# Performance work log

Measured on AMD Instinct MI355X. Metric: run time of the kernel, lower is better.

The kernel has to match this reference:

```python
import jax, jax.numpy as jnp
import numpy as np

NAF, NBF, DT = 64, 32, 1
B, GROUP = 2000, 100
P = B * GROUP

def _lin(key, din, dout):
    kw, kb = jax.random.split(key)
    return (jax.random.normal(kw, (din, dout), jnp.float32) * 0.02,
            jax.random.normal(kb, (dout,), jnp.float32) * 0.01)

def setup_inputs() -> dict:
    key = jax.random.key(0)
    ks = jax.random.split(key, 12)
    pairs = jax.random.normal(ks[0], (P, 2 * NAF + NBF), jnp.float32)
    idx_pairs = jnp.full((B,), GROUP, dtype=jnp.int32)
    ref_feats = jax.random.normal(ks[1], (B, 32), jnp.float32)
    aw, ab = _lin(ks[2], NAF, 128)
    bw, bb = _lin(ks[3], NBF, 128)
    p1w, p1b = _lin(ks[4], 384, 512)
    p2w, p2b = _lin(ks[5], 512, 256)
    p3w, p3b = _lin(ks[6], 256, 1024)
    f1w, f1b = _lin(ks[7], 1024, 512)
    f2w, f2b = _lin(ks[8], 512, 32)
    f3w, f3b = _lin(ks[9], 32, DT)
    return dict(pairs=pairs, idx_pairs=idx_pairs, ref_feats=ref_feats,
                aw=aw, ab=ab, bw=bw, bb=bb,
                p1w=p1w, p1b=p1b, p2w=p2w, p2b=p2b, p3w=p3w, p3b=p3b,
                f1w=f1w, f1b=f1b, f2w=f2w, f2b=f2b, f3w=f3w, f3b=f3b)

def reference(pairs, idx_pairs, ref_feats,
              aw, ab, bw, bb,
              p1w, p1b, p2w, p2b, p3w, p3b,
              f1w, f1b, f2w, f2b, f3w, f3b):
    relu = jax.nn.relu
    a1 = relu(pairs[:, :NAF] @ aw + ab)            # [P,128]
    a2 = relu(pairs[:, NAF:2 * NAF] @ aw + ab)     # [P,128]
    be = relu(pairs[:, 2 * NAF:] @ bw + bb)        # [P,128]
    h = jnp.concatenate([a1, a2, be], axis=1)      # [P,384]
    h = relu(h @ p1w + p1b)
    h = relu(h @ p2w + p2b)
    x = h @ p3w + p3b                              # [P,1024]
    nb = idx_pairs.shape[0]
    seg = jnp.repeat(jnp.arange(nb, dtype=jnp.int32), idx_pairs,
                     total_repeat_length=x.shape[0])
    sums = jax.ops.segment_sum(x, seg, num_segments=nb)
    h_pair = sums / idx_pairs[:, None].astype(x.dtype)  # segment mean [B,1024]
    h = relu(h_pair @ f1w + f1b)
    h = relu(h @ f2w + f2b)
    return h @ f3w + f3b                           # [B,1]
```

## Files before the change

kernel.cpp:

```cpp
#include <hip/hip_runtime.h>
#include <cstdint>
#include <cstddef>


typedef __bf16 bf16;
typedef __attribute__((ext_vector_type(8))) __bf16 bf16x8;
typedef __attribute__((ext_vector_type(4))) __bf16 bf16x4;
typedef __attribute__((ext_vector_type(4))) float floatx4;

#define GRP 100
#define NWIN 3125

#define WOFF_AW 0
#define WOFF_BW 8192
#define WOFF_P1 12288
#define WOFF_P2 208896
#define WOFF_P3 339968
#define WOFF_F1 602112
#define WOFF_F2 1126400
#define WOFF_HS 1142784

#define LSTR_P  168
#define LSTR_H  392
#define LSTR_H2 136
#define LSTR_MS 264

static __device__ __forceinline__ floatx4 mfma16(bf16x8 a, bf16x8 b, floatx4 c) {
  return __builtin_amdgcn_mfma_f32_16x16x32_bf16(a, b, c, 0, 0, 0);
}

static __device__ __forceinline__ void gload(floatx4& d, const bf16* p) {
  asm volatile("global_load_dwordx4 %0, %1, off" : "=v"(d) : "v"(p));
}
static __device__ __forceinline__ bf16x8 bc8(floatx4 v) {
  return __builtin_bit_cast(bf16x8, v);
}

#define VMW(N)                                         \
  do {                                                 \
    asm volatile("s_waitcnt vmcnt(" #N ")");           \
    __builtin_amdgcn_sched_barrier(0);                 \
  } while (0)

#define SYNCL()                                        \
  do {                                                 \
    asm volatile("s_waitcnt lgkmcnt(0)" ::: "memory"); \
    __builtin_amdgcn_s_barrier();                      \
  } while (0)

__global__ __launch_bounds__(256) void pack_lds(
    const float* __restrict__ aw, const float* __restrict__ bw,
    const float* __restrict__ p1w, const float* __restrict__ p2w,
    const float* __restrict__ p3w, const float* __restrict__ f1w,
    const float* __restrict__ f2w, bf16* __restrict__ wpk) {
  __shared__ float t[32][65];
  const int tid = threadIdx.x;
  int b = blockIdx.x;

  if (b < 550) {
    const float* src; int dstoff, K, N, tt;
    if (b < 4)        { src = aw;  dstoff = WOFF_AW; K = 64;   N = 128;  tt = b; }
    else if (b < 6)   { src = bw;  dstoff = WOFF_BW; K = 32;   N = 128;  tt = b - 4; }
    else if (b < 102) { src = p1w; dstoff = WOFF_P1; K = 384;  N = 512;  tt = b - 6; }
    else if (b < 166) { src = p2w; dstoff = WOFF_P2; K = 512;  N = 256;  tt = b - 102; }
    else if (b < 294) { src = p3w; dstoff = WOFF_P3; K = 256;  N = 1024; tt = b - 166; }
    else              { src = f1w; dstoff = WOFF_F1; K = 1024; N = 512;  tt = b - 294; }
    const int KT = K >> 5;
    const int kt = tt % KT;
    const int n0 = (tt / KT) * 64;
    for (int i = tid; i < 2048; i += 256) {
      int r = i >> 6, c = i & 63;
      t[r][c] = src[(size_t)(kt * 32 + r) * N + n0 + c];
    }
    __syncthreads();
    const int nc = n0 >> 7, nl0 = n0 & 127;
    bf16* dst = wpk + dstoff + ((size_t)(nc * KT + kt) * 128 + nl0) * 32;
    int o = tid * 8;
    int nl = o >> 5, kk = o & 31;
    bf16x8 v;
#pragma unroll
    for (int i = 0; i < 8; ++i) v[i] = (bf16)t[kk + i][nl];
    *(bf16x8*)(dst + nl * 32 + kk) = v;
  } else {
    const int kt = b - 550;
    for (int i = tid; i < 1024; i += 256) {
      int r = i >> 5, c = i & 31;
      t[r][c] = f2w[(size_t)(kt * 32 + r) * 32 + c];
    }
    __syncthreads();
    if (tid < 128) {
      int o = tid * 8;
      int nl = o >> 5, kk = o & 31;
      bf16x8 v;
#pragma unroll
      for (int i = 0; i < 8; ++i) v[i] = (bf16)t[kk + i][nl];
      *(bf16x8*)(wpk + WOFF_F2 + kt * 1024 + nl * 32 + kk) = v;
    }
  }
}

static __device__ __forceinline__ void kstep2(const bf16* __restrict__ Ab,
                                              int astride, int acol,
                                              const bf16* __restrict__ b0p,
                                              const bf16* __restrict__ b1p,
                                              floatx4* acc, int lm, int lq) {
  bf16x8 b0 = *(const bf16x8*)b0p;
  bf16x8 b1 = *(const bf16x8*)b1p;
#pragma unroll
  for (int mt = 0; mt < 4; ++mt) {
    bf16x8 a = *(const bf16x8*)(Ab + (mt * 16 + lm) * astride + acol + lq * 8);
    acc[mt * 2]     = mfma16(a, b0, acc[mt * 2]);
    acc[mt * 2 + 1] = mfma16(a, b1, acc[mt * 2 + 1]);
  }
}

static __device__ __forceinline__ void epi2(const floatx4* acc,
                                            const float* __restrict__ bias,
                                            bf16* dst, int dstride, int w,
                                            int lm, int lq) {
#pragma unroll
  for (int mt = 0; mt < 4; ++mt)
#pragma unroll
    for (int j = 0; j < 2; ++j) {
      int col = (w + 4 * j) * 16 + lm;
      float bv = bias[col];
      floatx4 c = acc[mt * 2 + j];
#pragma unroll
      for (int r = 0; r < 4; ++r) {
        float v = c[r] + bv;
        v = v > 0.f ? v : 0.f;
        dst[(mt * 16 + lq * 4 + r) * dstride + col] = (bf16)v;
      }
    }
}

static __device__ __forceinline__ void epi2v(const floatx4* acc, float bv0,
                                             float bv1, bf16* dst, int dstride,
                                             int w, int lm, int lq) {
#pragma unroll
  for (int mt = 0; mt < 4; ++mt)
#pragma unroll
    for (int j = 0; j < 2; ++j) {
      int col = (w + 4 * j) * 16 + lm;
      float bv = j ? bv1 : bv0;
      floatx4 c = acc[mt * 2 + j];
#pragma unroll
      for (int r = 0; r < 4; ++r) {
        float v = c[r] + bv;
        v = v > 0.f ? v : 0.f;
        dst[(mt * 16 + lq * 4 + r) * dstride + col] = (bf16)v;
      }
    }
}

__global__ __launch_bounds__(256, 2) void seg_kernel(
    const float* __restrict__ pairs, const float* __restrict__ ab,
    const float* __restrict__ bb, const float* __restrict__ p1b,
    const float* __restrict__ p2b, const bf16* __restrict__ wpk,
    float* __restrict__ hsum) {
  __shared__ __align__(16) bf16 hbuf[64 * LSTR_H];
  __shared__ __align__(16) bf16 pbuf[64 * LSTR_P];

  const int tid = threadIdx.x;
  const int w = tid >> 6;
  const int lane = tid & 63;
  const int lm = lane & 15;
  const int lq = lane >> 4;
  const int blk = blockIdx.x;

  {
    const float4* src = (const float4*)(pairs + (size_t)blk * (64 * 160));
    for (int i = tid; i < 64 * 40; i += 256) {
      int row = i / 40;
      int c4 = (i - row * 40) * 4;
      float4 v = src[i];
      bf16x4 o = {(bf16)v.x, (bf16)v.y, (bf16)v.z, (bf16)v.w};
      *(bf16x4*)(pbuf + row * LSTR_P + c4) = o;
    }
  }
  SYNCL();

  const floatx4 fz = {0.f, 0.f, 0.f, 0.f};
  floatx4 acc[8];
  floatx4 acc3[16];

#pragma unroll
  for (int t = 0; t < 8; ++t) acc[t] = fz;
#pragma unroll
  for (int kt = 0; kt < 2; ++kt)
    kstep2(pbuf, LSTR_P, kt * 32,
           wpk + WOFF_AW + ((size_t)(kt * 128 + w * 16 + lm)) * 32 + lq * 8,
           wpk + WOFF_AW + ((size_t)(kt * 128 + (w + 4) * 16 + lm)) * 32 + lq * 8,
           acc, lm, lq);
  epi2(acc, ab, hbuf, LSTR_H, w, lm, lq);
#pragma unroll
  for (int t = 0; t < 8; ++t) acc[t] = fz;
#pragma unroll
  for (int kt = 0; kt < 2; ++kt)
    kstep2(pbuf, LSTR_P, 64 + kt * 32,
           wpk + WOFF_AW + ((size_t)(kt * 128 + w * 16 + lm)) * 32 + lq * 8,
           wpk + WOFF_AW + ((size_t)(kt * 128 + (w + 4) * 16 + lm)) * 32 + lq * 8,
           acc, lm, lq);
  epi2(acc, ab, hbuf + 128, LSTR_H, w, lm, lq);
#pragma unroll
  for (int t = 0; t < 8; ++t) acc[t] = fz;
  kstep2(pbuf, LSTR_P, 128,
         wpk + WOFF_BW + ((size_t)(w * 16 + lm)) * 32 + lq * 8,
         wpk + WOFF_BW + ((size_t)((w + 4) * 16 + lm)) * 32 + lq * 8,
         acc, lm, lq);
  epi2(acc, bb, hbuf + 256, LSTR_H, w, lm, lq);

  float p1bv0[4], p1bv1[4], p2bv[4];
#pragma unroll
  for (int nc = 0; nc < 4; ++nc) {
    p1bv0[nc] = p1b[nc * 128 + w * 16 + lm];
    p1bv1[nc] = p1b[nc * 128 + (w + 4) * 16 + lm];
  }
#pragma unroll
  for (int s = 0; s < 4; ++s) p2bv[s] = p2b[w * 64 + s * 16 + lm];
  asm volatile("" : "+v"(p1bv0[0]), "+v"(p1bv0[1]), "+v"(p1bv0[2]),
                    "+v"(p1bv0[3]), "+v"(p1bv1[0]), "+v"(p1bv1[1]),
                    "+v"(p1bv1[2]), "+v"(p1bv1[3]), "+v"(p2bv[0]),
                    "+v"(p2bv[1]), "+v"(p2bv[2]), "+v"(p2bv[3]));

  const bf16* bp0 = wpk + WOFF_P1 + ((size_t)(w * 16 + lm)) * 32 + lq * 8;
  const bf16* bp2 = wpk + WOFF_P2 +
      ((size_t)(((w >> 1) * 16) * 128 + (w & 1) * 64 + lm)) * 32 + lq * 8;

  floatx4 p1r0[4], p1r1[4];
  floatx4 p2r[3][4];

#pragma unroll
  for (int q = 0; q < 3; ++q) {
    gload(p1r0[q], bp0 + (size_t)q * 4096);
    gload(p1r1[q], bp0 + (size_t)q * 4096 + 2048);
  }
  SYNCL();

#pragma unroll
  for (int t = 0; t < 16; ++t) acc3[t] = fz;

#pragma unroll
  for (int nc = 0; nc < 4; ++nc) {
#pragma unroll
    for (int t = 0; t < 8; ++t) acc[t] = fz;

    {
      bf16x8 an[2][4];
#pragma unroll
      for (int q = 0; q < 2; ++q)
#pragma unroll
        for (int mt = 0; mt < 4; ++mt)
          an[q][mt] = *(const bf16x8*)(hbuf + (mt * 16 + lm) * LSTR_H +
                                       q * 32 + lq * 8);
#pragma unroll
      for (int kt = 0; kt < 12; ++kt) {
        bf16x8 ac[4];
#pragma unroll
        for (int mt = 0; mt < 4; ++mt) ac[mt] = an[kt & 1][mt];
        if (kt < 10) {
#pragma unroll
          for (int mt = 0; mt < 4; ++mt)
            an[kt & 1][mt] = *(const bf16x8*)(hbuf + (mt * 16 + lm) * LSTR_H +
                                              (kt + 2) * 32 + lq * 8);
        }
        if (kt < 9) {
          gload(p1r0[(kt + 3) & 3], bp0 + (size_t)(nc * 12 + kt + 3) * 4096);
          gload(p1r1[(kt + 3) & 3],
                bp0 + (size_t)(nc * 12 + kt + 3) * 4096 + 2048);
        }
        if (kt < 9)       { VMW(6); }
        else if (kt == 9) { VMW(4); }
        else if (kt == 10){ VMW(2); }
        else              { VMW(0); }
        __builtin_amdgcn_s_setprio(1);
        bf16x8 b0 = bc8(p1r0[kt & 3]);
        bf16x8 b1 = bc8(p1r1[kt & 3]);
#pragma unroll
        for (int mt = 0; mt < 4; ++mt) {
          acc[mt * 2]     = mfma16(ac[mt], b0, acc[mt * 2]);
          acc[mt * 2 + 1] = mfma16(ac[mt], b1, acc[mt * 2 + 1]);
        }
        __builtin_amdgcn_s_setprio(0);
      }
    }

#pragma unroll
    for (int q = 0; q < 2; ++q)
#pragma unroll
      for (int j = 0; j < 4; ++j)
        gload(p2r[q][j], bp2 + (size_t)(nc * 4 + q) * 4096 + j * 512);

    SYNCL();
    epi2v(acc, p1bv0[nc], p1bv1[nc], pbuf, LSTR_H2, w, lm, lq);
    SYNCL();

    {
      bf16x8 an2[2][4];
#pragma unroll
      for (int q = 0; q < 2; ++q)
#pragma unroll
        for (int mt = 0; mt < 4; ++mt)
          an2[q][mt] = *(const bf16x8*)(pbuf + (mt * 16 + lm) * LSTR_H2 +
                                        q * 32 + lq * 8);
#pragma unroll
      for (int kt2 = 0; kt2 < 4; ++kt2) {
        bf16x8 ac[4];
#pragma unroll
        for (int mt = 0; mt < 4; ++mt) ac[mt] = an2[kt2 & 1][mt];
        if (kt2 < 2) {
#pragma unroll
          for (int mt = 0; mt < 4; ++mt)
            an2[kt2 & 1][mt] = *(const bf16x8*)(pbuf + (mt * 16 + lm) * LSTR_H2 +
                                                (kt2 + 2) * 32 + lq * 8);
#pragma unroll
          for (int j = 0; j < 4; ++j)
            gload(p2r[(kt2 + 2) % 3][j],
                  bp2 + (size_t)(nc * 4 + kt2 + 2) * 4096 + j * 512);
        }
        if (kt2 == 1) {
          const int ncn = (nc + 1) & 3;
#pragma unroll
          for (int q = 0; q < 3; ++q) {
            gload(p1r0[q], bp0 + (size_t)(ncn * 12 + q) * 4096);
            gload(p1r1[q], bp0 + (size_t)(ncn * 12 + q) * 4096 + 2048);
          }
        }
        if (kt2 == 0)      { VMW(8); }
        else if (kt2 == 1) { VMW(14); }
        else if (kt2 == 2) { VMW(10); }
        else               { VMW(6); }
        __builtin_amdgcn_s_setprio(1);
#pragma unroll
        for (int mt = 0; mt < 4; ++mt)
#pragma unroll
          for (int j = 0; j < 4; ++j)
            acc3[mt * 4 + j] =
                mfma16(ac[mt], bc8(p2r[kt2 % 3][j]), acc3[mt * 4 + j]);
        __builtin_amdgcn_s_setprio(0);
      }
    }
  }

  const int s0 = (64 * blk) / 100;
  const int sp = (s0 + 1) * 100 - 64 * blk;
  floatx4 msk[4];
#pragma unroll
  for (int mt = 0; mt < 4; ++mt)
#pragma unroll
    for (int r = 0; r < 4; ++r)
      msk[mt][r] = (mt * 16 + lq * 4 + r < sp) ? 1.f : 0.f;

#pragma unroll
  for (int s = 0; s < 4; ++s) {
    int cl = w * 64 + s * 16 + lm;
    float bv = p2bv[s];
    float tot = 0.f, cs0 = 0.f;
#pragma unroll
    for (int mt = 0; mt < 4; ++mt) {
      floatx4 c = acc3[mt * 4 + s];
#pragma unroll
      for (int r = 0; r < 4; ++r) {
        float v = c[r] + bv;
        v = v > 0.f ? v : 0.f;
        tot += v;
        cs0 = fmaf(v, msk[mt][r], cs0);
      }
    }
    float cs1 = tot - cs0;
    cs0 += __shfl_xor(cs0, 16, 64);
    cs0 += __shfl_xor(cs0, 32, 64);
    cs1 += __shfl_xor(cs1, 16, 64);
    cs1 += __shfl_xor(cs1, 32, 64);
    if (lq == 0) {
      hsum[(size_t)(2 * blk) * 256 + cl]     = cs0;
      hsum[(size_t)(2 * blk + 1) * 256 + cl] = cs1;
    }
  }
}

__global__ __launch_bounds__(512, 2) void tail_kernel(
    const bf16* __restrict__ wpk, const float* __restrict__ hsum,
    const int* __restrict__ idxp, const float* __restrict__ p3b,
    const float* __restrict__ f1b, const float* __restrict__ f2b,
    const float* __restrict__ f3w, const float* __restrict__ f3b,
    float* __restrict__ out) {
  __shared__ __align__(16) bf16 ms[16 * LSTR_MS];
  __shared__ __align__(16) bf16 hp[16 * 1032];
  __shared__ __align__(16) bf16 h2s[16 * 520];
  __shared__ __align__(16) bf16 h3s[16 * 40];

  const int tid = threadIdx.x;
  const int w = tid >> 6;
  const int lane = tid & 63;
  const int lm = lane & 15;
  const int lq = lane >> 4;
  const int r0 = blockIdx.x * 16;
  const floatx4 fz = {0.f, 0.f, 0.f, 0.f};

  for (int i = tid; i < 16 * 64; i += 512) {
    int row = i >> 6, c4 = i & 63;
    int seg = r0 + row;
    int b_lo = (100 * seg) >> 6;
    int b_hi = (100 * seg + 99) >> 6;
    float4 sa = {0.f, 0.f, 0.f, 0.f};
    for (int b = b_lo; b <= b_hi; ++b) {
      int slot = (64 * b >= 100 * seg) ? 0 : 1;
      float4 v = *(const float4*)(hsum + (size_t)(2 * b + slot) * 256 + c4 * 4);
      sa.x += v.x; sa.y += v.y; sa.z += v.z; sa.w += v.w;
    }
    float inv = 1.f / (float)idxp[seg];
    bf16x4 o = {(bf16)(sa.x * inv), (bf16)(sa.y * inv),
                (bf16)(sa.z * inv), (bf16)(sa.w * inv)};
    *(bf16x4*)(ms + row * LSTR_MS + c4 * 4) = o;
  }
  __syncthreads();

#pragma unroll
  for (int nt2 = 0; nt2 < 4; ++nt2) {
    floatx4 a2[2];
    a2[0] = fz; a2[1] = fz;
#pragma unroll
    for (int kt = 0; kt < 8; ++kt) {
      bf16x8 a = *(const bf16x8*)(ms + lm * LSTR_MS + kt * 32 + lq * 8);
#pragma unroll
      for (int j = 0; j < 2; ++j) {
        bf16x8 b = *(const bf16x8*)(wpk + WOFF_P3 +
            ((size_t)((w * 8 + kt) * 128 + (nt2 * 2 + j) * 16 + lm)) * 32 +
            lq * 8);
        a2[j] = mfma16(a, b, a2[j]);
      }
    }
#pragma unroll
    for (int j = 0; j < 2; ++j) {
      int col = w * 128 + (nt2 * 2 + j) * 16 + lm;
      float bv = p3b[col];
#pragma unroll
      for (int r = 0; r < 4; ++r)
        hp[(lq * 4 + r) * 1032 + col] = (bf16)(a2[j][r] + bv);
    }
  }
  __syncthreads();

  {
    floatx4 a4[4];
#pragma unroll
    for (int j = 0; j < 4; ++j) a4[j] = fz;
#pragma unroll 8
    for (int kt = 0; kt < 32; ++kt) {
      bf16x8 a = *(const bf16x8*)(hp + lm * 1032 + kt * 32 + lq * 8);
#pragma unroll
      for (int j = 0; j < 4; ++j) {
        bf16x8 b = *(const bf16x8*)(wpk + WOFF_F1 +
            ((size_t)(((w >> 1) * 32 + kt) * 128 + (w & 1) * 64 + j * 16 + lm)) * 32 +
            lq * 8);
        a4[j] = mfma16(a, b, a4[j]);
      }
    }
#pragma unroll
    for (int j = 0; j < 4; ++j) {
      int col = w * 64 + j * 16 + lm;
      float bv = f1b[col];
#pragma unroll
      for (int r = 0; r < 4; ++r) {
        float v = a4[j][r] + bv;
        v = v > 0.f ? v : 0.f;
        h2s[(lq * 4 + r) * 520 + col] = (bf16)v;
      }
    }
  }
  __syncthreads();

  if (w < 2) {
    floatx4 c2 = fz;
#pragma unroll
    for (int kt = 0; kt < 16; ++kt) {
      bf16x8 a = *(const bf16x8*)(h2s + lm * 520 + kt * 32 + lq * 8);
      bf16x8 b = *(const bf16x8*)(wpk + WOFF_F2 +
                    ((size_t)(kt * 32 + w * 16 + lm)) * 32 + lq * 8);
      c2 = mfma16(a, b, c2);
    }
    int col = w * 16 + lm;
    float bv = f2b[col];
#pragma unroll
    for (int r = 0; r < 4; ++r) {
      float v = c2[r] + bv;
      v = v > 0.f ? v : 0.f;
      h3s[(lq * 4 + r) * 40 + col] = (bf16)v;
    }
  }
  __syncthreads();
  if (w == 0) {
    float ps = 0.f;
#pragma unroll
    for (int jj = 0; jj < 8; ++jj)
      ps += (float)h3s[lm * 40 + lq * 8 + jj] * f3w[lq * 8 + jj];
    ps += __shfl_xor(ps, 16, 64);
    ps += __shfl_xor(ps, 32, 64);
    if (lq == 0) out[r0 + lm] = ps + f3b[0];
  }
}

extern "C" void kernel_launch(void* const* d_in, const int* in_sizes, int n_in,
                              void* d_out, int out_size, void* d_ws,
                              size_t ws_size, hipStream_t stream) {
  (void)in_sizes; (void)n_in; (void)out_size; (void)ws_size;
  const float* pairs = (const float*)d_in[0];
  const int*   idxp  = (const int*)d_in[1];
  const float* aw  = (const float*)d_in[3];
  const float* ab  = (const float*)d_in[4];
  const float* bw  = (const float*)d_in[5];
  const float* bb  = (const float*)d_in[6];
  const float* p1w = (const float*)d_in[7];
  const float* p1b = (const float*)d_in[8];
  const float* p2w = (const float*)d_in[9];
  const float* p2b = (const float*)d_in[10];
  const float* p3w = (const float*)d_in[11];
  const float* p3b = (const float*)d_in[12];
  const float* f1w = (const float*)d_in[13];
  const float* f1b = (const float*)d_in[14];
  const float* f2w = (const float*)d_in[15];
  const float* f2b = (const float*)d_in[16];
  const float* f3w = (const float*)d_in[17];
  const float* f3b = (const float*)d_in[18];

  bf16* wpk = (bf16*)d_ws;
  float* hsum = (float*)(wpk + WOFF_HS);

  pack_lds<<<566, 256, 0, stream>>>(aw, bw, p1w, p2w, p3w, f1w, f2w, wpk);
  seg_kernel<<<NWIN, 256, 0, stream>>>(pairs, ab, bb, p1b, p2b, wpk, hsum);
  tail_kernel<<<125, 512, 0, stream>>>(wpk, hsum, idxp, p3b, f1b, f2b, f3w,
                                       f3b, (float*)d_out);
}
```

Before: 399.5 us.

## Switch p1/p2 GEMMs in seg_kernel to 32x32x16 MFMA with repacked weights

Replaces the 16x16x32 bf16 MFMA tiles in the p1 and p2 layers of seg_kernel with 32x32x16 MFMA, so each wave computes 32-column tiles over 64 rows. The packing kernel gets a new weight layout for p1w and p2w, so each lane reads one contiguous 16-byte fragment per MFMA operand. The intent is fewer MFMA issues and better operand reuse per instruction, with fewer LDS reads per FLOP. In exchange, the accumulators are larger (floatx16), which raises register pressure, and the epilogue row mapping and segment reduction had to be rewritten.

```diff
diff --git a/kernel.cpp b/kernel.cpp
--- a/kernel.cpp
+++ b/kernel.cpp
@@ -7,6 +7,7 @@
 typedef __attribute__((ext_vector_type(8))) __bf16 bf16x8;
 typedef __attribute__((ext_vector_type(4))) __bf16 bf16x4;
 typedef __attribute__((ext_vector_type(4))) float floatx4;
+typedef __attribute__((ext_vector_type(16))) float floatx16;
 
 #define GRP 100
 #define NWIN 3125
@@ -28,6 +29,9 @@
 static __device__ __forceinline__ floatx4 mfma16(bf16x8 a, bf16x8 b, floatx4 c) {
   return __builtin_amdgcn_mfma_f32_16x16x32_bf16(a, b, c, 0, 0, 0);
 }
+static __device__ __forceinline__ floatx16 mfma32(bf16x8 a, bf16x8 b, floatx16 c) {
+  return __builtin_amdgcn_mfma_f32_32x32x16_bf16(a, b, c, 0, 0, 0);
+}
 
 static __device__ __forceinline__ void gload(floatx4& d, const bf16* p) {
   asm volatile("global_load_dwordx4 %0, %1, off" : "=v"(d) : "v"(p));
@@ -59,10 +63,11 @@
 
   if (b < 550) {
     const float* src; int dstoff, K, N, tt;
+    bool newf = false;
     if (b < 4)        { src = aw;  dstoff = WOFF_AW; K = 64;   N = 128;  tt = b; }
     else if (b < 6)   { src = bw;  dstoff = WOFF_BW; K = 32;   N = 128;  tt = b - 4; }
-    else if (b < 102) { src = p1w; dstoff = WOFF_P1; K = 384;  N = 512;  tt = b - 6; }
-    else if (b < 166) { src = p2w; dstoff = WOFF_P2; K = 512;  N = 256;  tt = b - 102; }
+    else if (b < 102) { src = p1w; dstoff = WOFF_P1; K = 384;  N = 512;  tt = b - 6;   newf = true; }
+    else if (b < 166) { src = p2w; dstoff = WOFF_P2; K = 512;  N = 256;  tt = b - 102; newf = true; }
     else if (b < 294) { src = p3w; dstoff = WOFF_P3; K = 256;  N = 1024; tt = b - 166; }
     else              { src = f1w; dstoff = WOFF_F1; K = 1024; N = 512;  tt = b - 294; }
     const int KT = K >> 5;
@@ -73,14 +78,26 @@
       t[r][c] = src[(size_t)(kt * 32 + r) * N + n0 + c];
     }
     __syncthreads();
-    const int nc = n0 >> 7, nl0 = n0 & 127;
-    bf16* dst = wpk + dstoff + ((size_t)(nc * KT + kt) * 128 + nl0) * 32;
-    int o = tid * 8;
-    int nl = o >> 5, kk = o & 31;
-    bf16x8 v;
-#pragma unroll
-    for (int i = 0; i < 8; ++i) v[i] = (bf16)t[kk + i][nl];
-    *(bf16x8*)(dst + nl * 32 + kk) = v;
+    if (newf) {
+      const int cpp = tid & 63, rb = tid >> 6;
+      const int g = (n0 >> 5) + (cpp >> 5);
+      const int c = cpp & 31;
+      bf16x8 v;
+#pragma unroll
+      for (int i = 0; i < 8; ++i) v[i] = (bf16)t[rb * 8 + i][cpp];
+      *(bf16x8*)(wpk + dstoff +
+                 (((size_t)g * KT + kt) * 2 + (rb >> 1)) * 512 +
+                 (c + 32 * (rb & 1)) * 8) = v;
+    } else {
+      const int nc = n0 >> 7, nl0 = n0 & 127;
+      bf16* dst = wpk + dstoff + ((size_t)(nc * KT + kt) * 128 + nl0) * 32;
+      int o = tid * 8;
+      int nl = o >> 5, kk = o & 31;
+      bf16x8 v;
+#pragma unroll
+      for (int i = 0; i < 8; ++i) v[i] = (bf16)t[kk + i][nl];
+      *(bf16x8*)(dst + nl * 32 + kk) = v;
+    }
   } else {
     const int kt = b - 550;
     for (int i = tid; i < 1024; i += 256) {
@@ -134,25 +151,6 @@
     }
 }
 
-static __device__ __forceinline__ void epi2v(const floatx4* acc, float bv0,
-                                             float bv1, bf16* dst, int dstride,
-                                             int w, int lm, int lq) {
-#pragma unroll
-  for (int mt = 0; mt < 4; ++mt)
-#pragma unroll
-    for (int j = 0; j < 2; ++j) {
-      int col = (w + 4 * j) * 16 + lm;
-      float bv = j ? bv1 : bv0;
-      floatx4 c = acc[mt * 2 + j];
-#pragma unroll
-      for (int r = 0; r < 4; ++r) {
-        float v = c[r] + bv;
-        v = v > 0.f ? v : 0.f;
-        dst[(mt * 16 + lq * 4 + r) * dstride + col] = (bf16)v;
-      }
-    }
-}
-
 __global__ __launch_bounds__(256, 2) void seg_kernel(
     const float* __restrict__ pairs, const float* __restrict__ ab,
     const float* __restrict__ bb, const float* __restrict__ p1b,
@@ -166,6 +164,10 @@
   const int lane = tid & 63;
   const int lm = lane & 15;
   const int lq = lane >> 4;
+  const int l31 = lane & 31;
+  const int hi = lane >> 5;
+  const int hi8 = hi * 8;
+  const int ln8 = lane * 8;
   const int blk = blockIdx.x;
 
   {
@@ -181,8 +183,9 @@
   SYNCL();
 
   const floatx4 fz = {0.f, 0.f, 0.f, 0.f};
+  const floatx16 fz16 = {0.f, 0.f, 0.f, 0.f, 0.f, 0.f, 0.f, 0.f,
+                         0.f, 0.f, 0.f, 0.f, 0.f, 0.f, 0.f, 0.f};
   floatx4 acc[8];
-  floatx4 acc3[16];
 
 #pragma unroll
   for (int t = 0; t < 8; ++t) acc[t] = fz;
@@ -210,64 +213,61 @@
          acc, lm, lq);
   epi2(acc, bb, hbuf + 256, LSTR_H, w, lm, lq);
 
-  float p1bv0[4], p1bv1[4], p2bv[4];
-#pragma unroll
-  for (int nc = 0; nc < 4; ++nc) {
-    p1bv0[nc] = p1b[nc * 128 + w * 16 + lm];
-    p1bv1[nc] = p1b[nc * 128 + (w + 4) * 16 + lm];
-  }
-#pragma unroll
-  for (int s = 0; s < 4; ++s) p2bv[s] = p2b[w * 64 + s * 16 + lm];
-  asm volatile("" : "+v"(p1bv0[0]), "+v"(p1bv0[1]), "+v"(p1bv0[2]),
-                    "+v"(p1bv0[3]), "+v"(p1bv1[0]), "+v"(p1bv1[1]),
-                    "+v"(p1bv1[2]), "+v"(p1bv1[3]), "+v"(p2bv[0]),
-                    "+v"(p2bv[1]), "+v"(p2bv[2]), "+v"(p2bv[3]));
-
-  const bf16* bp0 = wpk + WOFF_P1 + ((size_t)(w * 16 + lm)) * 32 + lq * 8;
-  const bf16* bp2 = wpk + WOFF_P2 +
-      ((size_t)(((w >> 1) * 16) * 128 + (w & 1) * 64 + lm)) * 32 + lq * 8;
+  float p1bv[4], p2bv[2];
+#pragma unroll
+  for (int nc = 0; nc < 4; ++nc) p1bv[nc] = p1b[nc * 128 + w * 32 + l31];
+  p2bv[0] = p2b[w * 32 + l31];
+  p2bv[1] = p2b[(w + 4) * 32 + l31];
+  asm volatile("" : "+v"(p1bv[0]), "+v"(p1bv[1]), "+v"(p1bv[2]),
+                    "+v"(p1bv[3]), "+v"(p2bv[0]), "+v"(p2bv[1]));
 
   floatx4 p1r0[4], p1r1[4];
   floatx4 p2r[3][4];
+  floatx16 acc3[4];
 
 #pragma unroll
   for (int q = 0; q < 3; ++q) {
-    gload(p1r0[q], bp0 + (size_t)q * 4096);
-    gload(p1r1[q], bp0 + (size_t)q * 4096 + 2048);
+    gload(p1r0[q], wpk + WOFF_P1 + (((size_t)w * 12 + q) * 2 + 0) * 512 + ln8);
+    gload(p1r1[q], wpk + WOFF_P1 + (((size_t)w * 12 + q) * 2 + 1) * 512 + ln8);
   }
   SYNCL();
 
 #pragma unroll
-  for (int t = 0; t < 16; ++t) acc3[t] = fz;
+  for (int t = 0; t < 4; ++t) acc3[t] = fz16;
 
 #pragma unroll
   for (int nc = 0; nc < 4; ++nc) {
-#pragma unroll
-    for (int t = 0; t < 8; ++t) acc[t] = fz;
+    const int gw = nc * 4 + w;
+    floatx16 acc2[2];
+    acc2[0] = fz16; acc2[1] = fz16;
 
     {
       bf16x8 an[2][4];
 #pragma unroll
       for (int q = 0; q < 2; ++q)
 #pragma unroll
-        for (int mt = 0; mt < 4; ++mt)
-          an[q][mt] = *(const bf16x8*)(hbuf + (mt * 16 + lm) * LSTR_H +
-                                       q * 32 + lq * 8);
+        for (int rg = 0; rg < 2; ++rg)
+#pragma unroll
+          for (int h = 0; h < 2; ++h)
+            an[q][rg * 2 + h] = *(const bf16x8*)(
+                hbuf + (rg * 32 + l31) * LSTR_H + q * 32 + h * 16 + hi8);
 #pragma unroll
       for (int kt = 0; kt < 12; ++kt) {
-        bf16x8 ac[4];
-#pragma unroll
-        for (int mt = 0; mt < 4; ++mt) ac[mt] = an[kt & 1][mt];
+        bf16x8 a00 = an[kt & 1][0], a01 = an[kt & 1][1];
+        bf16x8 a10 = an[kt & 1][2], a11 = an[kt & 1][3];
         if (kt < 10) {
 #pragma unroll
-          for (int mt = 0; mt < 4; ++mt)
-            an[kt & 1][mt] = *(const bf16x8*)(hbuf + (mt * 16 + lm) * LSTR_H +
-                                              (kt + 2) * 32 + lq * 8);
+          for (int rg = 0; rg < 2; ++rg)
+#pragma unroll
+            for (int h = 0; h < 2; ++h)
+              an[kt & 1][rg * 2 + h] = *(const bf16x8*)(
+                  hbuf + (rg * 32 + l31) * LSTR_H + (kt + 2) * 32 + h * 16 + hi8);
         }
         if (kt < 9) {
-          gload(p1r0[(kt + 3) & 3], bp0 + (size_t)(nc * 12 + kt + 3) * 4096);
+          gload(p1r0[(kt + 3) & 3],
+                wpk + WOFF_P1 + (((size_t)gw * 12 + kt + 3) * 2 + 0) * 512 + ln8);
           gload(p1r1[(kt + 3) & 3],
-                bp0 + (size_t)(nc * 12 + kt + 3) * 4096 + 2048);
+                wpk + WOFF_P1 + (((size_t)gw * 12 + kt + 3) * 2 + 1) * 512 + ln8);
         }
         if (kt < 9)       { VMW(6); }
         else if (kt == 9) { VMW(4); }
@@ -276,23 +276,38 @@
         __builtin_amdgcn_s_setprio(1);
         bf16x8 b0 = bc8(p1r0[kt & 3]);
         bf16x8 b1 = bc8(p1r1[kt & 3]);
-#pragma unroll
-        for (int mt = 0; mt < 4; ++mt) {
-          acc[mt * 2]     = mfma16(ac[mt], b0, acc[mt * 2]);
-          acc[mt * 2 + 1] = mfma16(ac[mt], b1, acc[mt * 2 + 1]);
+        acc2[0] = mfma32(a00, b0, acc2[0]);
+        acc2[1] = mfma32(a10, b0, acc2[1]);
+        acc2[0] = mfma32(a01, b1, acc2[0]);
+        acc2[1] = mfma32(a11, b1, acc2[1]);
+        __builtin_amdgcn_s_setprio(0);
+      }
+    }
+
+#pragma unroll
+    for (int q = 0; q < 2; ++q)
+#pragma unroll
+      for (int cg = 0; cg < 2; ++cg)
+#pragma unroll
+        for (int h = 0; h < 2; ++h)
+          gload(p2r[q][cg * 2 + h],
+                wpk + WOFF_P2 +
+                    (((size_t)(cg ? w + 4 : w) * 16 + nc * 4 + q) * 2 + h) * 512 +
+                    ln8);
+
+    SYNCL();
+    {
+      float bv = p1bv[nc];
+#pragma unroll
+      for (int rg = 0; rg < 2; ++rg)
+#pragma unroll
+        for (int r = 0; r < 16; ++r) {
+          float v = acc2[rg][r] + bv;
+          v = v > 0.f ? v : 0.f;
+          int row = rg * 32 + (r & 3) + 8 * (r >> 2) + 4 * hi;
+          pbuf[row * LSTR_H2 + w * 32 + l31] = (bf16)v;
         }
-        __builtin_amdgcn_s_setprio(0);
-      }
-    }
-
-#pragma unroll
-    for (int q = 0; q < 2; ++q)
-#pragma unroll
-      for (int j = 0; j < 4; ++j)
-        gload(p2r[q][j], bp2 + (size_t)(nc * 4 + q) * 4096 + j * 512);
-
-    SYNCL();
-    epi2v(acc, p1bv0[nc], p1bv1[nc], pbuf, LSTR_H2, w, lm, lq);
+    }
     SYNCL();
 
     {
@@ -300,30 +315,40 @@
 #pragma unroll
       for (int q = 0; q < 2; ++q)
 #pragma unroll
-        for (int mt = 0; mt < 4; ++mt)
-          an2[q][mt] = *(const bf16x8*)(pbuf + (mt * 16 + lm) * LSTR_H2 +
-                                        q * 32 + lq * 8);
+        for (int rg = 0; rg < 2; ++rg)
+#pragma unroll
+          for (int h = 0; h < 2; ++h)
+            an2[q][rg * 2 + h] = *(const bf16x8*)(
+                pbuf + (rg * 32 + l31) * LSTR_H2 + q * 32 + h * 16 + hi8);
 #pragma unroll
       for (int kt2 = 0; kt2 < 4; ++kt2) {
         bf16x8 ac[4];
 #pragma unroll
-        for (int mt = 0; mt < 4; ++mt) ac[mt] = an2[kt2 & 1][mt];
+        for (int f = 0; f < 4; ++f) ac[f] = an2[kt2 & 1][f];
         if (kt2 < 2) {
 #pragma unroll
-          for (int mt = 0; mt < 4; ++mt)
-            an2[kt2 & 1][mt] = *(const bf16x8*)(pbuf + (mt * 16 + lm) * LSTR_H2 +
-                                                (kt2 + 2) * 32 + lq * 8);
-#pragma unroll
-          for (int j = 0; j < 4; ++j)
-            gload(p2r[(kt2 + 2) % 3][j],
-                  bp2 + (size_t)(nc * 4 + kt2 + 2) * 4096 + j * 512);
+          for (int rg = 0; rg < 2; ++rg)
+#pragma unroll
+            for (int h = 0; h < 2; ++h)
+              an2[kt2 & 1][rg * 2 + h] = *(const bf16x8*)(
+                  pbuf + (rg * 32 + l31) * LSTR_H2 + (kt2 + 2) * 32 + h * 16 + hi8);
+#pragma unroll
+          for (int cg = 0; cg < 2; ++cg)
+#pragma unroll
+            for (int h = 0; h < 2; ++h)
+              gload(p2r[(kt2 + 2) % 3][cg * 2 + h],
+                    wpk + WOFF_P2 +
+                        (((size_t)(cg ? w + 4 : w) * 16 + nc * 4 + kt2 + 2) * 2 + h) *
+                            512 + ln8);
         }
         if (kt2 == 1) {
-          const int ncn = (nc + 1) & 3;
+          const int gn = ((nc + 1) & 3) * 4 + w;
 #pragma unroll
           for (int q = 0; q < 3; ++q) {
-            gload(p1r0[q], bp0 + (size_t)(ncn * 12 + q) * 4096);
-            gload(p1r1[q], bp0 + (size_t)(ncn * 12 + q) * 4096 + 2048);
+            gload(p1r0[q],
+                  wpk + WOFF_P1 + (((size_t)gn * 12 + q) * 2 + 0) * 512 + ln8);
+            gload(p1r1[q],
+                  wpk + WOFF_P1 + (((size_t)gn * 12 + q) * 2 + 1) * 512 + ln8);
           }
         }
         if (kt2 == 0)      { VMW(8); }
@@ -332,11 +357,14 @@
         else               { VMW(6); }
         __builtin_amdgcn_s_setprio(1);
 #pragma unroll
-        for (int mt = 0; mt < 4; ++mt)
-#pragma unroll
-          for (int j = 0; j < 4; ++j)
-            acc3[mt * 4 + j] =
-                mfma16(ac[mt], bc8(p2r[kt2 % 3][j]), acc3[mt * 4 + j]);
+        for (int h = 0; h < 2; ++h) {
+          bf16x8 b0 = bc8(p2r[kt2 % 3][0 * 2 + h]);
+          bf16x8 b1 = bc8(p2r[kt2 % 3][1 * 2 + h]);
+          acc3[0] = mfma32(ac[0 * 2 + h], b0, acc3[0]);
+          acc3[1] = mfma32(ac[0 * 2 + h], b1, acc3[1]);
+          acc3[2] = mfma32(ac[1 * 2 + h], b0, acc3[2]);
+          acc3[3] = mfma32(ac[1 * 2 + h], b1, acc3[3]);
+        }
         __builtin_amdgcn_s_setprio(0);
       }
     }
@@ -344,37 +372,28 @@
 
   const int s0 = (64 * blk) / 100;
   const int sp = (s0 + 1) * 100 - 64 * blk;
-  floatx4 msk[4];
-#pragma unroll
-  for (int mt = 0; mt < 4; ++mt)
-#pragma unroll
-    for (int r = 0; r < 4; ++r)
-      msk[mt][r] = (mt * 16 + lq * 4 + r < sp) ? 1.f : 0.f;
-
-#pragma unroll
-  for (int s = 0; s < 4; ++s) {
-    int cl = w * 64 + s * 16 + lm;
-    float bv = p2bv[s];
+
+#pragma unroll
+  for (int cg = 0; cg < 2; ++cg) {
+    float bv = p2bv[cg];
     float tot = 0.f, cs0 = 0.f;
 #pragma unroll
-    for (int mt = 0; mt < 4; ++mt) {
-      floatx4 c = acc3[mt * 4 + s];
-#pragma unroll
-      for (int r = 0; r < 4; ++r) {
-        float v = c[r] + bv;
+    for (int rg = 0; rg < 2; ++rg)
+#pragma unroll
+      for (int r = 0; r < 16; ++r) {
+        float v = acc3[rg * 2 + cg][r] + bv;
         v = v > 0.f ? v : 0.f;
         tot += v;
-        cs0 = fmaf(v, msk[mt][r], cs0);
-      }
-    }
+        int row = rg * 32 + (r & 3) + 8 * (r >> 2) + 4 * hi;
+        cs0 += (row < sp) ? v : 0.f;
+      }
     float cs1 = tot - cs0;
-    cs0 += __shfl_xor(cs0, 16, 64);
     cs0 += __shfl_xor(cs0, 32, 64);
-    cs1 += __shfl_xor(cs1, 16, 64);
     cs1 += __shfl_xor(cs1, 32, 64);
-    if (lq == 0) {
-      hsum[(size_t)(2 * blk) * 256 + cl]     = cs0;
-      hsum[(size_t)(2 * blk + 1) * 256 + cl] = cs1;
+    if (lane < 32) {
+      int col = (cg ? w + 4 : w) * 32 + lane;
+      hsum[(size_t)(2 * blk) * 256 + col]     = cs0;
+      hsum[(size_t)(2 * blk + 1) * 256 + col] = cs1;
     }
   }
 }
```

Result: faster. 386.0 us, median of 2 (-3.4%).
